# Kernel optimization log

Hardware: AMD Instinct MI355X
Metric: run time of the kernel (lower is better)

## Reference

```python
import jax, jax.numpy as jnp
import numpy as np


def setup_inputs() -> dict:
    key = jax.random.key(0)
    k1, k2, k3, k4 = jax.random.split(key, 4)
    B, C, H, W = 4, 256, 64, 64
    Va = jax.random.normal(k1, (B, C, H, W), jnp.float32)
    Vb = jax.random.normal(k2, (B, C, H, W), jnp.float32)
    # nn.Linear(C, C, bias=False) weight, used as x @ W^T
    W_linear = jax.random.normal(k3, (C, C), jnp.float32) * 0.05
    # nn.Conv2d(C, 1, 1, bias=False) weight, init normal_(0, 0.01)
    W_gate = jax.random.normal(k4, (C,), jnp.float32) * 0.01
    return {"Va_output": Va, "Vb_output": Vb, "W_linear": W_linear,
            "W_gate": W_gate, "input_size": 512}


def reference(Va_output, Vb_output, W_linear, W_gate, input_size):
    B, C, H, W = Vb_output.shape
    A = H * W  # all_dim
    Va_flat = Va_output.reshape(B, C, A)  # [B, C, A]
    Vb_flat = Vb_output.reshape(B, C, A)
    # linear on transposed A-major tokens: Va_t @ W_linear^T -> [B, A, C]
    Va_corr = jnp.einsum('bca,dc->bad', Va_flat, W_linear)
    # correlation matrix S = Va_corr @ Vb_flat -> [B, A, A]
    S = jnp.einsum('bac,can->ban'[:3] + 'c,c' if False else 'bac,cn', Va_corr, Vb_flat) if False else jnp.einsum('bac,bcn->ban', Va_corr, Vb_flat)
    # S_c = softmax(S, dim=1); S_r = softmax(S^T, dim=1) = softmax(S, axis=2)^T
    S_c = jax.nn.softmax(S, axis=1)
    S_r = jnp.swapaxes(jax.nn.softmax(S, axis=2), 1, 2)
    Vb_att = jnp.einsum('bca,ban->bcn', Va_flat, S_r).reshape(B, C, H, W)
    Va_att = jnp.einsum('bca,ban->bcn', Vb_flat, S_c).reshape(B, C, H, W)
    # 1x1 gate conv (C -> 1, no bias) + sigmoid
    Va_mask = jax.nn.sigmoid(jnp.einsum('bchw,c->bhw', Va_att, W_gate))[:, None]
    Vb_mask = jax.nn.sigmoid(jnp.einsum('bchw,c->bhw', Vb_att, W_gate))[:, None]
    Va_out = jnp.concatenate([Va_att * Va_mask, Va_output], axis=1)  # [B, 2C, H, W]
    Vb_out = jnp.concatenate([Vb_att * Vb_mask, Vb_output], axis=1)
    return (Va_out, Vb_out, input_size)
```

## Files before the change

kernel.cpp:

```cpp
#include <hip/hip_runtime.h>

typedef _Float16 f16;
typedef f16 f16x8 __attribute__((ext_vector_type(8)));
typedef float f32x4 __attribute__((ext_vector_type(4)));
typedef short b16x8 __attribute__((ext_vector_type(8)));
typedef unsigned short u16;
typedef u16 u16x4 __attribute__((ext_vector_type(4)));

#define MFMA_F16(a,b,c)  __builtin_amdgcn_mfma_f32_16x16x32_f16((a),(b),(c),0,0,0)
#define MFMA_BF16(a,b,c) __builtin_amdgcn_mfma_f32_16x16x32_bf16((a),(b),(c),0,0,0)

static __device__ __forceinline__ u16 bf16rn(float f) {
    unsigned u = __builtin_bit_cast(unsigned, f);
    u += 0x7FFFu + ((u >> 16) & 1u);
    return (u16)(u >> 16);
}

typedef const __attribute__((address_space(1))) unsigned int* gas_p;
typedef __attribute__((address_space(3))) unsigned int* las_p;
static __device__ __forceinline__ void gll16(const void* g, void* l) {
    __builtin_amdgcn_global_load_lds((gas_p)g, (las_p)l, 16, 0, 0);
}

static constexpr int B_ = 4, C_ = 256, A_ = 4096;
static constexpr int CA   = C_ * A_;
static constexpr int BCA  = B_ * CA;
static constexpr int OUT_T = B_ * 2 * CA;
static constexpr size_t WS_Va16 = 0;
static constexpr size_t WS_Vb16 = WS_Va16 + (size_t)BCA;
static constexpr size_t WS_VaT  = WS_Vb16 + (size_t)BCA;
static constexpr size_t WS_VbT  = WS_VaT  + (size_t)BCA;
static constexpr size_t WS_Q1   = WS_VbT  + (size_t)BCA;
static constexpr size_t WS_W16  = WS_Q1   + (size_t)BCA;
static constexpr size_t WS_HALFS = WS_W16 + (size_t)(C_ * C_);

static constexpr float M0 = 48.0f;

__global__ void coatt_convw(const float* __restrict__ W, f16* __restrict__ W16) {
    int i = blockIdx.x * 256 + threadIdx.x;
    W16[i] = (f16)W[i];
}

__global__ void coatt_transpose(const float* __restrict__ Va,
                                const float* __restrict__ Vb,
                                u16* __restrict__ ws) {
    __shared__ f16 tile[64][72];
    int z = blockIdx.z; int b = z >> 1; int which = z & 1;
    const float* src = which ? Vb : Va;
    u16* cm = ws + (which ? WS_Vb16 : WS_Va16);
    f16* am = (f16*)(ws + (which ? WS_VbT : WS_VaT));
    int a0 = blockIdx.x * 64, c0 = blockIdx.y * 64;
    int t = threadIdx.x;
    int r = t >> 2, q = t & 3;

    const float* sp = src + (size_t)(b * C_ + c0 + r) * A_ + a0 + q * 16;
    f16 h[16] __attribute__((aligned(16)));
    u16 hb[16] __attribute__((aligned(16)));
#pragma unroll
    for (int i = 0; i < 4; ++i) {
        float4 v = *(const float4*)(sp + i * 4);
        h[i*4+0] = (f16)v.x; h[i*4+1] = (f16)v.y;
        h[i*4+2] = (f16)v.z; h[i*4+3] = (f16)v.w;
        hb[i*4+0] = bf16rn(v.x); hb[i*4+1] = bf16rn(v.y);
        hb[i*4+2] = bf16rn(v.z); hb[i*4+3] = bf16rn(v.w);
    }
    u16* cp = cm + (size_t)(b * C_ + c0 + r) * A_ + a0 + q * 16;
    *(u16x4*)(cp)      = *(const u16x4*)&hb[0];
    *(u16x4*)(cp + 4)  = *(const u16x4*)&hb[4];
    *(u16x4*)(cp + 8)  = *(const u16x4*)&hb[8];
    *(u16x4*)(cp + 12) = *(const u16x4*)&hb[12];
#pragma unroll
    for (int i = 0; i < 16; ++i) tile[r][q * 16 + i] = h[i];
    __syncthreads();
    f16 ht[16] __attribute__((aligned(16)));
#pragma unroll
    for (int i = 0; i < 16; ++i) ht[i] = tile[q * 16 + i][r];
    f16* ap = am + (size_t)(b * A_ + a0 + r) * C_ + c0 + q * 16;
    *(f16x8*)(ap)     = *(const f16x8*)&ht[0];
    *(f16x8*)(ap + 8) = *(const f16x8*)&ht[8];
}

__global__ __launch_bounds__(256) void coatt_q1(const f16* __restrict__ vat,
                                                const f16* __restrict__ w16,
                                                f16* __restrict__ q1) {
    int b = blockIdx.y; int a0 = blockIdx.x * 64;
    int tid = threadIdx.x, wave = tid >> 6, lane = tid & 63;
    int m = lane & 15, quad = lane >> 4;

    const f16* Ap = vat + (size_t)(b * A_ + a0 + wave * 16 + m) * C_ + quad * 8;
    f16x8 af[8];
#pragma unroll
    for (int kc = 0; kc < 8; ++kc) af[kc] = *(const f16x8*)(Ap + kc * 32);

    f32x4 acc[16];
#pragma unroll
    for (int t = 0; t < 16; ++t) acc[t] = (f32x4){0.f, 0.f, 0.f, 0.f};

#pragma unroll
    for (int kc = 0; kc < 8; ++kc) {
#pragma unroll
        for (int t = 0; t < 16; ++t) {
            f16x8 bf = *(const f16x8*)(w16 + (size_t)(t * 16 + m) * C_ + kc * 32 + quad * 8);
            acc[t] = MFMA_F16(af[kc], bf, acc[t]);
        }
    }
#pragma unroll
    for (int t = 0; t < 16; ++t) {
#pragma unroll
        for (int r = 0; r < 4; ++r) {
            int arow = a0 + wave * 16 + quad * 4 + r;
            q1[(size_t)(b * A_ + arow) * C_ + t * 16 + m] = (f16)acc[t][r];
        }
    }
}

__global__ __launch_bounds__(256, 2) void coatt_flash(const u16* __restrict__ ws,
                                                      const float* __restrict__ Wgate,
                                                      float* __restrict__ dout) {
    __shared__ __align__(16) char smem[78848];
    char* Klds = smem;
    char* Vlds = smem + 34816;
    char* Plds = smem + 69632;
    float* Olds = (float*)smem;
    float* Lsum = (float*)(smem + 69632);
    float* Gsum = (float*)(smem + 69632 + 512);

    int att = blockIdx.z, b = blockIdx.y;
    int n0 = blockIdx.x * 64;
    const f16 *Qp, *Kp; const u16* Vp; float* outp;
    if (att == 0) {
        Qp = (const f16*)(ws + WS_Q1)  + (size_t)b * CA;
        Kp = (const f16*)(ws + WS_VbT) + (size_t)b * CA;
        Vp = ws + WS_Va16 + (size_t)b * CA;
        outp = dout + (size_t)OUT_T + (size_t)b * 2 * CA;
    } else {
        Qp = (const f16*)(ws + WS_VbT) + (size_t)b * CA;
        Kp = (const f16*)(ws + WS_Q1)  + (size_t)b * CA;
        Vp = ws + WS_Vb16 + (size_t)b * CA;
        outp = dout + (size_t)b * 2 * CA;
    }

    int tid = threadIdx.x, wave = tid >> 6, lane = tid & 63;
    int i = wave >> 1, j = wave & 1;
    int m = lane & 15, quad = lane >> 4;

    f16x8 qf[2][8];
#pragma unroll
    for (int qt = 0; qt < 2; ++qt) {
        const f16* qr = Qp + (size_t)(n0 + i * 32 + qt * 16 + m) * C_ + quad * 8;
#pragma unroll
        for (int kc = 0; kc < 8; ++kc) qf[qt][kc] = *(const f16x8*)(qr + kc * 32);
    }

    f32x4 Oacc[2][8];
#pragma unroll
    for (int qt = 0; qt < 2; ++qt)
#pragma unroll
        for (int ct = 0; ct < 8; ++ct) Oacc[qt][ct] = (f32x4){0.f, 0.f, 0.f, 0.f};
    float lpart[2] = {0.f, 0.f};

    for (int kb = 0; kb < 64; ++kb) {
        int key0 = kb * 64;
        {
            const f16* kg = Kp + (size_t)(key0 + 2 * wave) * C_ + lane * 8;
            char* kl = Klds + wave * 1088;
#pragma unroll
            for (int ii = 0; ii < 8; ++ii)
                gll16(kg + ii * 2048, kl + ii * 4352);
            const u16* vg = Vp + (size_t)(wave * 8 + (lane >> 3)) * A_ + key0 + (lane & 7) * 8;
            char* vl = Vlds + wave * 1088;
#pragma unroll
            for (int ii = 0; ii < 8; ++ii)
                gll16(vg + (size_t)ii * 32 * A_, vl + ii * 4352);
        }
        __syncthreads();

        f32x4 Sc[2][2];
#pragma unroll
        for (int kt = 0; kt < 2; ++kt)
#pragma unroll
            for (int qt = 0; qt < 2; ++qt) Sc[kt][qt] = (f32x4){0.f, 0.f, 0.f, 0.f};
#pragma unroll
        for (int kc = 0; kc < 8; ++kc) {
            f16x8 kf[2];
#pragma unroll
            for (int kt = 0; kt < 2; ++kt) {
                int kl_ = j * 32 + kt * 16 + m;
                kf[kt] = *(const f16x8*)(Klds + (kl_ >> 1) * 1088 + (kl_ & 1) * 512 +
                                         kc * 64 + quad * 16);
            }
#pragma unroll
            for (int kt = 0; kt < 2; ++kt)
#pragma unroll
                for (int qt = 0; qt < 2; ++qt)
                    Sc[kt][qt] = MFMA_F16(kf[kt], qf[qt][kc], Sc[kt][qt]);
        }

#pragma unroll
        for (int qt = 0; qt < 2; ++qt) {
            int qg = i * 32 + qt * 16 + m;
#pragma unroll
            for (int kt = 0; kt < 2; ++kt) {
                u16x4 pk;
                float s4 = 0.f;
#pragma unroll
                for (int r = 0; r < 4; ++r) {
                    float p = __expf(Sc[kt][qt][r] - M0);
                    s4 += p;
                    pk[r] = bf16rn(p);
                }
                lpart[qt] += s4;
                *(u16x4*)(Plds + qg * 144 + (j * 32 + kt * 16 + quad * 4) * 2) = pk;
            }
        }
        __syncthreads();

#pragma unroll
        for (int kt = 0; kt < 2; ++kt) {
            b16x8 pf[2];
#pragma unroll
            for (int qt = 0; qt < 2; ++qt) {
                int qg = i * 32 + qt * 16 + m;
                pf[qt] = *(const b16x8*)(Plds + qg * 144 + kt * 64 + quad * 16);
            }
#pragma unroll
            for (int ct = 0; ct < 8; ++ct) {
                int c = j * 128 + ct * 16 + m;
                b16x8 vf = *(const b16x8*)(Vlds + (c >> 3) * 1088 + (c & 7) * 128 +
                                           kt * 64 + quad * 16);
#pragma unroll
                for (int qt = 0; qt < 2; ++qt)
                    Oacc[qt][ct] = MFMA_BF16(pf[qt], vf, Oacc[qt][ct]);
            }
        }
        __syncthreads();
    }

#pragma unroll
    for (int qt = 0; qt < 2; ++qt) {
        float v = lpart[qt];
        v += __shfl_xor(v, 16);
        v += __shfl_xor(v, 32);
        lpart[qt] = v;
    }
    if (lane < 16) {
#pragma unroll
        for (int qt = 0; qt < 2; ++qt)
            Lsum[j * 64 + i * 32 + qt * 16 + lane] = lpart[qt];
    }
    __syncthreads();
    float inv[2][4];
#pragma unroll
    for (int qt = 0; qt < 2; ++qt)
#pragma unroll
        for (int r = 0; r < 4; ++r) {
            int q = i * 32 + qt * 16 + quad * 4 + r;
            inv[qt][r] = 1.0f / (Lsum[q] + Lsum[64 + q]);
        }
    float gp[2][4] = {{0.f,0.f,0.f,0.f},{0.f,0.f,0.f,0.f}};
#pragma unroll
    for (int ct = 0; ct < 8; ++ct) {
        float w = Wgate[j * 128 + ct * 16 + m];
#pragma unroll
        for (int qt = 0; qt < 2; ++qt)
#pragma unroll
            for (int r = 0; r < 4; ++r) {
                float o = Oacc[qt][ct][r] * inv[qt][r];
                Oacc[qt][ct][r] = o;
                gp[qt][r] += o * w;
            }
    }
#pragma unroll
    for (int qt = 0; qt < 2; ++qt)
#pragma unroll
        for (int r = 0; r < 4; ++r) {
            float v = gp[qt][r];
            v += __shfl_xor(v, 1); v += __shfl_xor(v, 2);
            v += __shfl_xor(v, 4); v += __shfl_xor(v, 8);
            gp[qt][r] = v;
        }
    if (m == 0) {
#pragma unroll
        for (int qt = 0; qt < 2; ++qt)
#pragma unroll
            for (int r = 0; r < 4; ++r)
                Gsum[j * 64 + i * 32 + qt * 16 + quad * 4 + r] = gp[qt][r];
    }
    __syncthreads();
#pragma unroll
    for (int qt = 0; qt < 2; ++qt)
#pragma unroll
        for (int r = 0; r < 4; ++r) {
            int q = i * 32 + qt * 16 + quad * 4 + r;
            float g = Gsum[q] + Gsum[64 + q];
            float msk = 1.0f / (1.0f + __expf(-g));
#pragma unroll
            for (int ct = 0; ct < 8; ++ct) Oacc[qt][ct][r] *= msk;
        }

    for (int hf = 0; hf < 2; ++hf) {
        __syncthreads();
        if (j == hf) {
#pragma unroll
            for (int ct = 0; ct < 8; ++ct)
#pragma unroll
                for (int qt = 0; qt < 2; ++qt)
#pragma unroll
                    for (int r = 0; r < 4; ++r)
                        Olds[(ct * 16 + m) * 68 + i * 32 + qt * 16 + quad * 4 + r] =
                            Oacc[qt][ct][r];
        }
        __syncthreads();
#pragma unroll
        for (int ii = 0; ii < 8; ++ii) {
            int ci = tid + ii * 256;
            int c = ci >> 4, ch = (ci & 15) * 4;
            float4 v = *(const float4*)(Olds + c * 68 + ch);
            *(float4*)(outp + (size_t)(hf * 128 + c) * A_ + n0 + ch) = v;
        }
    }
}

__global__ void coatt_copy(const float* __restrict__ Va, const float* __restrict__ Vb,
                           const int* __restrict__ psz, float* __restrict__ dout) {
    int base = blockIdx.x * 256 + threadIdx.x;
    const float4* va4 = (const float4*)Va;
    const float4* vb4 = (const float4*)Vb;
    float4* out4 = (float4*)dout;
#pragma unroll
    for (int i = 0; i < 4; ++i) {
        int idx = base + i * 524288;
        int t = idx >> 20;
        int r = idx & 1048575;
        int b = r >> 18;
        int rr = r & 262143;
        float4 v = t ? vb4[r] : va4[r];
        out4[(size_t)t * 2097152 + (size_t)b * 524288 + 262144 + rr] = v;
    }
    if (base == 0) dout[16777216] = (float)(*psz);
}

extern "C" void kernel_launch(void* const* d_in, const int* in_sizes, int n_in,
                              void* d_out, int out_size, void* d_ws, size_t ws_size,
                              hipStream_t stream) {
    const float* Va = (const float*)d_in[0];
    const float* Vb = (const float*)d_in[1];
    const float* Wl = (const float*)d_in[2];
    const float* Wg = (const float*)d_in[3];
    const int* psz  = (const int*)d_in[4];
    float* out = (float*)d_out;
    u16* ws = (u16*)d_ws;

    if (ws_size < WS_HALFS * sizeof(u16)) return;

    coatt_convw<<<256, 256, 0, stream>>>(Wl, (f16*)(ws + WS_W16));
    coatt_transpose<<<dim3(64, 4, 8), 256, 0, stream>>>(Va, Vb, ws);
    coatt_q1<<<dim3(64, 4), 256, 0, stream>>>((const f16*)(ws + WS_VaT),
                                              (const f16*)(ws + WS_W16),
                                              (f16*)(ws + WS_Q1));
    coatt_flash<<<dim3(64, 4, 2), 256, 0, stream>>>(ws, Wg, out);
    coatt_copy<<<2048, 256, 0, stream>>>(Va, Vb, psz, out);
}
```

Baseline: 288.4 us.

## Fuse passthrough copy into transpose and restage V tile with padded rows

The separate copy kernel that wrote Va/Vb into the second half of each output is removed. The transpose kernel now writes the fp32 values it already loads straight to the output, and the scalar input_size write moves into the weight-conversion kernel. This saves one kernel launch and a full re-read of both inputs. Separately, the flash kernel's V tile is now loaded through registers into a row-padded LDS layout (144-byte rows) instead of global_load_lds, and the K and V strides are repacked to change LDS bank behaviour and staging.

```diff
diff --git a/kernel.cpp b/kernel.cpp
--- a/kernel.cpp
+++ b/kernel.cpp
@@ -36,14 +36,16 @@
 
 static constexpr float M0 = 48.0f;
 
-__global__ void coatt_convw(const float* __restrict__ W, f16* __restrict__ W16) {
+__global__ void coatt_convw(const float* __restrict__ W, f16* __restrict__ W16,
+                            const int* __restrict__ psz, float* __restrict__ dout) {
     int i = blockIdx.x * 256 + threadIdx.x;
     W16[i] = (f16)W[i];
+    if (i == 0) dout[16777216] = (float)(*psz);
 }
 
 __global__ void coatt_transpose(const float* __restrict__ Va,
                                 const float* __restrict__ Vb,
-                                u16* __restrict__ ws) {
+                                u16* __restrict__ ws, float* __restrict__ dout) {
     __shared__ f16 tile[64][72];
     int z = blockIdx.z; int b = z >> 1; int which = z & 1;
     const float* src = which ? Vb : Va;
@@ -54,11 +56,14 @@
     int r = t >> 2, q = t & 3;
 
     const float* sp = src + (size_t)(b * C_ + c0 + r) * A_ + a0 + q * 16;
+    float* rp = dout + (size_t)which * OUT_T + (size_t)b * 2 * CA + CA
+                + (size_t)(c0 + r) * A_ + a0 + q * 16;
     f16 h[16] __attribute__((aligned(16)));
     u16 hb[16] __attribute__((aligned(16)));
 #pragma unroll
     for (int i = 0; i < 4; ++i) {
         float4 v = *(const float4*)(sp + i * 4);
+        *(float4*)(rp + i * 4) = v;
         h[i*4+0] = (f16)v.x; h[i*4+1] = (f16)v.y;
         h[i*4+2] = (f16)v.z; h[i*4+3] = (f16)v.w;
         hb[i*4+0] = bf16rn(v.x); hb[i*4+1] = bf16rn(v.y);
@@ -117,13 +122,13 @@
 __global__ __launch_bounds__(256, 2) void coatt_flash(const u16* __restrict__ ws,
                                                       const float* __restrict__ Wgate,
                                                       float* __restrict__ dout) {
-    __shared__ __align__(16) char smem[78848];
+    __shared__ __align__(16) char smem[80384];
     char* Klds = smem;
-    char* Vlds = smem + 34816;
-    char* Plds = smem + 69632;
+    char* Vlds = smem + 33280;
+    char* Plds = smem + 70144;
     float* Olds = (float*)smem;
-    float* Lsum = (float*)(smem + 69632);
-    float* Gsum = (float*)(smem + 69632 + 512);
+    float* Lsum = (float*)(smem + 79360);
+    float* Gsum = (float*)(smem + 79360 + 512);
 
     int att = blockIdx.z, b = blockIdx.y;
     int n0 = blockIdx.x * 64;
@@ -152,6 +157,9 @@
         for (int kc = 0; kc < 8; ++kc) qf[qt][kc] = *(const f16x8*)(qr + kc * 32);
     }
 
+    const u16* vgBase = Vp + (size_t)(tid >> 3) * A_ + (tid & 7) * 8;
+    char* vlBase = Vlds + (tid >> 3) * 144 + (tid & 7) * 16;
+
     f32x4 Oacc[2][8];
 #pragma unroll
     for (int qt = 0; qt < 2; ++qt)
@@ -163,15 +171,20 @@
         int key0 = kb * 64;
         {
             const f16* kg = Kp + (size_t)(key0 + 2 * wave) * C_ + lane * 8;
-            char* kl = Klds + wave * 1088;
+            char* kl = Klds + wave * 1040;
 #pragma unroll
             for (int ii = 0; ii < 8; ++ii)
-                gll16(kg + ii * 2048, kl + ii * 4352);
-            const u16* vg = Vp + (size_t)(wave * 8 + (lane >> 3)) * A_ + key0 + (lane & 7) * 8;
-            char* vl = Vlds + wave * 1088;
+                gll16(kg + ii * 2048, kl + ii * 4160);
+        }
+        {
+            const u16* vg = vgBase + key0;
+            uint4 vt[8];
 #pragma unroll
             for (int ii = 0; ii < 8; ++ii)
-                gll16(vg + (size_t)ii * 32 * A_, vl + ii * 4352);
+                vt[ii] = *(const uint4*)(vg + (size_t)ii * 32 * A_);
+#pragma unroll
+            for (int ii = 0; ii < 8; ++ii)
+                *(uint4*)(vlBase + ii * 32 * 144) = vt[ii];
         }
         __syncthreads();
 
@@ -186,7 +199,7 @@
 #pragma unroll
             for (int kt = 0; kt < 2; ++kt) {
                 int kl_ = j * 32 + kt * 16 + m;
-                kf[kt] = *(const f16x8*)(Klds + (kl_ >> 1) * 1088 + (kl_ & 1) * 512 +
+                kf[kt] = *(const f16x8*)(Klds + (kl_ >> 1) * 1040 + (kl_ & 1) * 512 +
                                          kc * 64 + quad * 16);
             }
 #pragma unroll
@@ -226,8 +239,7 @@
 #pragma unroll
             for (int ct = 0; ct < 8; ++ct) {
                 int c = j * 128 + ct * 16 + m;
-                b16x8 vf = *(const b16x8*)(Vlds + (c >> 3) * 1088 + (c & 7) * 128 +
-                                           kt * 64 + quad * 16);
+                b16x8 vf = *(const b16x8*)(Vlds + c * 144 + kt * 64 + quad * 16);
 #pragma unroll
                 for (int qt = 0; qt < 2; ++qt)
                     Oacc[qt][ct] = MFMA_BF16(pf[qt], vf, Oacc[qt][ct]);
@@ -319,25 +331,6 @@
             *(float4*)(outp + (size_t)(hf * 128 + c) * A_ + n0 + ch) = v;
         }
     }
-}
-
-__global__ void coatt_copy(const float* __restrict__ Va, const float* __restrict__ Vb,
-                           const int* __restrict__ psz, float* __restrict__ dout) {
-    int base = blockIdx.x * 256 + threadIdx.x;
-    const float4* va4 = (const float4*)Va;
-    const float4* vb4 = (const float4*)Vb;
-    float4* out4 = (float4*)dout;
-#pragma unroll
-    for (int i = 0; i < 4; ++i) {
-        int idx = base + i * 524288;
-        int t = idx >> 20;
-        int r = idx & 1048575;
-        int b = r >> 18;
-        int rr = r & 262143;
-        float4 v = t ? vb4[r] : va4[r];
-        out4[(size_t)t * 2097152 + (size_t)b * 524288 + 262144 + rr] = v;
-    }
-    if (base == 0) dout[16777216] = (float)(*psz);
 }
 
 extern "C" void kernel_launch(void* const* d_in, const int* in_sizes, int n_in,
@@ -353,11 +346,10 @@
 
     if (ws_size < WS_HALFS * sizeof(u16)) return;
 
-    coatt_convw<<<256, 256, 0, stream>>>(Wl, (f16*)(ws + WS_W16));
-    coatt_transpose<<<dim3(64, 4, 8), 256, 0, stream>>>(Va, Vb, ws);
+    coatt_convw<<<256, 256, 0, stream>>>(Wl, (f16*)(ws + WS_W16), psz, out);
+    coatt_transpose<<<dim3(64, 4, 8), 256, 0, stream>>>(Va, Vb, ws, out);
     coatt_q1<<<dim3(64, 4), 256, 0, stream>>>((const f16*)(ws + WS_VaT),
                                               (const f16*)(ws + WS_W16),
                                               (f16*)(ws + WS_Q1));
     coatt_flash<<<dim3(64, 4, 2), 256, 0, stream>>>(ws, Wg, out);
-    coatt_copy<<<2048, 256, 0, stream>>>(Va, Vb, psz, out);
-}
+}
```

New measurement: 328.0 us. +13.8%, slower.
